# Optimization experiments

Hardware: AMD Instinct MI355X
Metric: run time of the kernel (lower is better)

The kernel has to match this reference:

```python
import jax, jax.numpy as jnp
import numpy as np
from jax import lax

INPUT_DIM = 1024
DICT_SIZE = 16384
K = 32
BATCH = 4096


def setup_inputs() -> dict:
    key = jax.random.key(0)
    k1, k2, k3 = jax.random.split(key, 3)
    x = jax.random.normal(k1, (BATCH, INPUT_DIM), dtype=jnp.float32)
    # kaiming-uniform-ish init for encoder
    bound_enc = float(np.sqrt(6.0 / INPUT_DIM))
    W_enc = jax.random.uniform(k2, (DICT_SIZE, INPUT_DIM), dtype=jnp.float32,
                               minval=-bound_enc, maxval=bound_enc)
    b_enc = jnp.zeros((DICT_SIZE,), dtype=jnp.float32)
    bound_dec = float(np.sqrt(6.0 / DICT_SIZE))
    W_dec = jax.random.uniform(k3, (INPUT_DIM, DICT_SIZE), dtype=jnp.float32,
                               minval=-bound_dec, maxval=bound_dec)
    # normalize decoder columns to unit norm (dim=0), as in _init_weights
    W_dec = W_dec / (jnp.linalg.norm(W_dec, axis=0, keepdims=True) + 1e-12)
    b_dec = jnp.zeros((INPUT_DIM,), dtype=jnp.float32)
    return {"x": x, "W_enc": W_enc, "b_enc": b_enc, "W_dec": W_dec, "b_dec": b_dec}


def reference(x, W_enc, b_enc, W_dec, b_dec):
    batch = x.shape[0]
    # encode: F.linear(x - b_dec, W_enc, b_enc)
    pre_acts = jnp.einsum('bi,di->bd', x - b_dec, W_enc) + b_enc  # [B, D]
    relu_acts = jnp.maximum(pre_acts, 0.0)
    # batch top-k: keep top (k * batch) activations globally
    flat = relu_acts.reshape(-1)
    total_k = min(K * batch, flat.shape[0])
    top_vals, _ = lax.top_k(flat, total_k)
    threshold = top_vals[-1]  # == kthvalue(numel - total_k + 1)
    features = relu_acts * (relu_acts >= threshold).astype(relu_acts.dtype)
    # decode: F.linear(features, W_dec, b_dec)
    reconstructed = jnp.einsum('bd,id->bi', features, W_dec) + b_dec  # [B, I]
    diff = reconstructed - x
    reconstruction_loss = jnp.mean(diff * diff)
    sparsity_loss = jnp.asarray(0.0, dtype=x.dtype)
    loss = reconstruction_loss
    l0 = jnp.mean(jnp.sum((features > 0).astype(jnp.float32), axis=-1))
    return (reconstructed, features, loss, reconstruction_loss, sparsity_loss, l0)
```

## Files before the change

### kernel.cpp

```cpp
#include <hip/hip_runtime.h>
#include <cstdint>
#include <cstddef>

#define BATCH   4096
#define INDIM   1024
#define DICT    16384
#define TOTK    (32 * 4096)
#define NFEAT   ((size_t)BATCH * DICT)
#define DELTA   3e-2f
#define BAND    0.2f
#define PS_RANK (TOTK / 32)

#define NB2       4096
#define FBINS     2048
#define HCOPIES   64
#define CAND_CAP  (1u << 19)
#define BCAP      256u
#define ZLOC_CAP  2048u
#define CLOC_CAP  3072
#define C2_CAP    65536u
#define HASH_SZ   32768u
#define ROW_CAP   512
#define ZBINS     2048

#define PSH_OFF   0ull
#define FH_OFF    16384ull
#define ZHH_OFF   24576ull
#define SCAL_OFF  32768ull
#define H1_OFF    36864ull
#define ROWC_OFF  40960ull
#define HASH_OFF  65536ull
#define FBH_OFF   524288ull
#define MEMSET0   1572864ull
#define CANDI_OFF (2ull << 20)
#define CANDB_OFF (4ull << 20)
#define C2I_OFF   (6ull << 20)
#define C2V_OFF   ((6ull << 20) + 262144)
#define ENT_OFF   (7ull << 20)
#define AHI_OFF   (24ull << 20)
#define BHI_OFF   (32ull << 20)
#define WT_OFF    (24ull << 20)
#define WS_NEED   (88ull << 20)

typedef __attribute__((ext_vector_type(8))) short short8;
typedef __attribute__((ext_vector_type(4))) float f32x4;

#define GL2LDS16(g, l) __builtin_amdgcn_global_load_lds( \
    (const __attribute__((address_space(1))) void*)(g), \
    (__attribute__((address_space(3))) void*)(l), 16, 0, 0)

__device__ inline ushort bf16_rne_u(float a) {
    unsigned u = __float_as_uint(a);
    return (ushort)((u + 0x7FFFu + ((u >> 16) & 1u)) >> 16);
}

__device__ inline int fshift_calc(unsigned BL, unsigned BH) {
    const unsigned range = BH - BL;
    int s = 0;
    while ((range >> s) > (unsigned)FBINS) ++s;
    return s;
}

__global__ __launch_bounds__(256) void split_kernel(
    const float* __restrict__ x, const float* __restrict__ W,
    const float* __restrict__ b_dec,
    ushort* __restrict__ Ahi, ushort* __restrict__ Bhi)
{
    const size_t NA = (size_t)BATCH * INDIM / 4;
    const size_t NB = (size_t)DICT * INDIM / 4;
    const size_t stride = (size_t)gridDim.x * blockDim.x;
    for (size_t i = (size_t)blockIdx.x * blockDim.x + threadIdx.x; i < NA + NB; i += stride) {
        float4 v;
        ushort* hp;
        if (i < NA) {
            v = reinterpret_cast<const float4*>(x)[i];
            const float4 bd = reinterpret_cast<const float4*>(b_dec)[i & (INDIM / 4 - 1)];
            v.x -= bd.x; v.y -= bd.y; v.z -= bd.z; v.w -= bd.w;
            hp = Ahi + i * 4;
        } else {
            v = reinterpret_cast<const float4*>(W)[i - NA];
            hp = Bhi + (i - NA) * 4;
        }
        ushort4 h;
        h.x = bf16_rne_u(v.x);
        h.y = bf16_rne_u(v.y);
        h.z = bf16_rne_u(v.z);
        h.w = bf16_rne_u(v.w);
        *reinterpret_cast<ushort4*>(hp) = h;
    }
}

__global__ __launch_bounds__(256) void presample_mfma(
    const ushort* __restrict__ Ahi, const ushort* __restrict__ Bhi,
    const float* __restrict__ b_enc, unsigned* __restrict__ pshist)
{
    __shared__ __align__(16) ushort As[128 * 64];
    __shared__ __align__(16) ushort Bs[128 * 64];
    __shared__ unsigned hls[NB2];
    const int tid = threadIdx.x;
    const int lane = tid & 63, wid = tid >> 6;
    const int n0 = blockIdx.x * 128;
    const int m0 = 0;
    const int wm = wid >> 1, wn = wid & 1;

    for (int i = tid; i < NB2; i += 256) hls[i] = 0;

    f32x4 acc[4][4];
#pragma unroll
    for (int i = 0; i < 4; ++i)
#pragma unroll
        for (int j = 0; j < 4; ++j) acc[i][j] = (f32x4){0.f, 0.f, 0.f, 0.f};

    const int srow = wid * 8 + (lane >> 3);
    const int schunk = (lane & 7) ^ (lane >> 3);
    const size_t abase = (size_t)(m0 + srow) * INDIM + schunk * 8;
    const size_t bbase = (size_t)(n0 + srow) * INDIM + schunk * 8;

    for (int t = 0; t < 16; ++t) {
        const int koff = t * 64;
#pragma unroll
        for (int i = 0; i < 4; ++i) {
            GL2LDS16(Ahi + abase + koff + (size_t)i * 32 * INDIM, &As[(i * 32 + wid * 8) * 64]);
            GL2LDS16(Bhi + bbase + koff + (size_t)i * 32 * INDIM, &Bs[(i * 32 + wid * 8) * 64]);
        }
        __syncthreads();
#pragma unroll
        for (int kq2 = 0; kq2 < 2; ++kq2) {
            short8 af[4], bf[4];
#pragma unroll
            for (int f = 0; f < 4; ++f) {
                const int ra = wm * 64 + f * 16 + (lane & 15);
                const int ca = (kq2 * 4 + (lane >> 4)) ^ (ra & 7);
                af[f] = *reinterpret_cast<const short8*>(&As[ra * 64 + ca * 8]);
                const int rb = wn * 64 + f * 16 + (lane & 15);
                const int cb = (kq2 * 4 + (lane >> 4)) ^ (rb & 7);
                bf[f] = *reinterpret_cast<const short8*>(&Bs[rb * 64 + cb * 8]);
            }
#pragma unroll
            for (int fm = 0; fm < 4; ++fm)
#pragma unroll
                for (int fn = 0; fn < 4; ++fn)
                    acc[fm][fn] = __builtin_amdgcn_mfma_f32_16x16x32_bf16(
                        af[fm], bf[fn], acc[fm][fn], 0, 0, 0);
        }
        __syncthreads();
    }

    const int ccol0 = n0 + wn * 64;
#pragma unroll
    for (int fm = 0; fm < 4; ++fm) {
#pragma unroll
        for (int fn = 0; fn < 4; ++fn) {
            const int col = ccol0 + fn * 16 + (lane & 15);
            const float be = b_enc[col];
#pragma unroll
            for (int r = 0; r < 4; ++r) {
                const float val = fmaxf(acc[fm][fn][r] + be, 0.f);
                if (val > 0.f) atomicAdd(&hls[__float_as_uint(val) >> 19], 1u);
            }
        }
    }
    __syncthreads();
    for (int i = tid; i < NB2; i += 256)
        if (hls[i]) atomicAdd(&pshist[i], hls[i]);
}

__global__ __launch_bounds__(1024) void presample_find(const unsigned* __restrict__ pshist,
                                                       unsigned* __restrict__ scal)
{
    __shared__ unsigned tot[NB2];
    __shared__ unsigned tsum[1024];
    __shared__ unsigned suffix[1024];
    const int t = threadIdx.x;
    unsigned s = 0;
#pragma unroll
    for (int i = 0; i < 4; ++i) {
        const int b = t * 4 + i;
        const unsigned v = pshist[b];
        tot[b] = v;
        s += v;
    }
    tsum[t] = s;
    __syncthreads();
    if (t == 0) {
        unsigned run = 0;
        for (int i = 1023; i >= 0; --i) { suffix[i] = run; run += tsum[i]; }
    }
    __syncthreads();
    unsigned cum = suffix[t];
    for (int i = 3; i >= 0; --i) {
        const unsigned b = (unsigned)(t * 4 + i);
        const unsigned nb = cum + tot[b];
        if (cum < PS_RANK && nb >= PS_RANK) {
            const float blo = __uint_as_float(b << 19);
            const float bhi = __uint_as_float((b + 1) << 19);
            scal[20] = __float_as_uint(fmaxf(blo - BAND, 1e-30f));
            scal[21] = __float_as_uint(bhi + BAND);
        }
        cum = nb;
    }
}

__global__ __launch_bounds__(256) void encode_main(
    const ushort* __restrict__ Ahi, const ushort* __restrict__ Bhi,
    const float* __restrict__ b_enc, unsigned* __restrict__ scal,
    unsigned* __restrict__ fhist, unsigned* __restrict__ candI,
    unsigned* __restrict__ candB)
{
    __shared__ __align__(16) ushort As[128 * 64];
    __shared__ __align__(16) ushort Bs[128 * 64];
    __shared__ unsigned fh[FBINS];
    __shared__ unsigned ci[BCAP];
    __shared__ unsigned cb[BCAP];
    __shared__ unsigned lcnt, labv, sbase;
    const int tid = threadIdx.x;
    const int lane = tid & 63, wid = tid >> 6;
    const int flat = blockIdx.y * gridDim.x + blockIdx.x;
    const int n0 = ((flat & 7) * 16 + ((flat >> 3) & 15)) * 128;
    const int m0 = (flat >> 7) * 128;
    const int wm = wid >> 1, wn = wid & 1;

    for (int i = tid; i < FBINS; i += 256) fh[i] = 0;
    if (tid == 0) { lcnt = 0; labv = 0; }

    const unsigned BLb = scal[20], BHb = scal[21];
    const float BLf = __uint_as_float(BLb);
    const int fs = fshift_calc(BLb, BHb);

    f32x4 acc[4][4];
#pragma unroll
    for (int i = 0; i < 4; ++i)
#pragma unroll
        for (int j = 0; j < 4; ++j) acc[i][j] = (f32x4){0.f, 0.f, 0.f, 0.f};

    const int srow = wid * 8 + (lane >> 3);
    const int schunk = (lane & 7) ^ (lane >> 3);
    const size_t abase = (size_t)(m0 + srow) * INDIM + schunk * 8;
    const size_t bbase = (size_t)(n0 + srow) * INDIM + schunk * 8;

    for (int t = 0; t < 16; ++t) {
        const int koff = t * 64;
#pragma unroll
        for (int i = 0; i < 4; ++i) {
            GL2LDS16(Ahi + abase + koff + (size_t)i * 32 * INDIM, &As[(i * 32 + wid * 8) * 64]);
            GL2LDS16(Bhi + bbase + koff + (size_t)i * 32 * INDIM, &Bs[(i * 32 + wid * 8) * 64]);
        }
        __syncthreads();
#pragma unroll
        for (int kq2 = 0; kq2 < 2; ++kq2) {
            short8 af[4], bf[4];
#pragma unroll
            for (int f = 0; f < 4; ++f) {
                const int ra = wm * 64 + f * 16 + (lane & 15);
                const int ca = (kq2 * 4 + (lane >> 4)) ^ (ra & 7);
                af[f] = *reinterpret_cast<const short8*>(&As[ra * 64 + ca * 8]);
                const int rb = wn * 64 + f * 16 + (lane & 15);
                const int cbx = (kq2 * 4 + (lane >> 4)) ^ (rb & 7);
                bf[f] = *reinterpret_cast<const short8*>(&Bs[rb * 64 + cbx * 8]);
            }
#pragma unroll
            for (int fm = 0; fm < 4; ++fm)
#pragma unroll
                for (int fn = 0; fn < 4; ++fn)
                    acc[fm][fn] = __builtin_amdgcn_mfma_f32_16x16x32_bf16(
                        af[fm], bf[fn], acc[fm][fn], 0, 0, 0);
        }
        __syncthreads();
    }

    const int crow0 = m0 + wm * 64;
    const int ccol0 = n0 + wn * 64;
#pragma unroll
    for (int fm = 0; fm < 4; ++fm) {
#pragma unroll
        for (int fn = 0; fn < 4; ++fn) {
            const int col = ccol0 + fn * 16 + (lane & 15);
            const float be = b_enc[col];
#pragma unroll
            for (int r = 0; r < 4; ++r) {
                const int row = crow0 + fm * 16 + (lane >> 4) * 4 + r;
                const float val = fmaxf(acc[fm][fn][r] + be, 0.f);
                if (val >= BLf) {
                    const unsigned u = __float_as_uint(val);
                    if (u < BHb) atomicAdd(&fh[min((u - BLb) >> fs, (unsigned)(FBINS - 1))], 1u);
                    else atomicAdd(&labv, 1u);
                    const unsigned p = atomicAdd(&lcnt, 1u);
                    if (p < BCAP) {
                        ci[p] = (unsigned)(row * DICT + col);
                        cb[p] = u;
                    }
                }
            }
        }
    }
    __syncthreads();
    for (int i = tid; i < FBINS; i += 256)
        if (fh[i]) atomicAdd(&fhist[i], fh[i]);
    if (tid == 0) {
        if (labv) atomicAdd(&scal[16], labv);
        const unsigned n = min(lcnt, BCAP);
        if (lcnt > BCAP) atomicExch(&scal[17], 1u);
        sbase = atomicAdd(&scal[2], n);
    }
    __syncthreads();
    const unsigned n = min(lcnt, BCAP);
    const unsigned gb = sbase;
    for (unsigned k = tid; k < n; k += 256) {
        const unsigned g = gb + k;
        if (g < CAND_CAP) { candI[g] = ci[k]; candB[g] = cb[k]; }
        else atomicExch(&scal[17], 1u);
    }
}

__global__ __launch_bounds__(1024) void findfine_a(const unsigned* __restrict__ fhist,
                                                   unsigned* __restrict__ scal)
{
    __shared__ unsigned fhl[FBINS];
    __shared__ unsigned tsum[1024];
    __shared__ unsigned suffix[1024];
    __shared__ unsigned sfb;
    const int t = threadIdx.x;
    fhl[t * 2] = fhist[t * 2];
    fhl[t * 2 + 1] = fhist[t * 2 + 1];
    tsum[t] = fhl[t * 2] + fhl[t * 2 + 1];
    if (t == 0) sfb = 0xFFFFFFFFu;
    __syncthreads();
    if (t == 0) {
        unsigned run = 0;
        for (int i = 1023; i >= 0; --i) { suffix[i] = run; run += tsum[i]; }
    }
    __syncthreads();
    const unsigned aboveBH = scal[16];
    unsigned cum = aboveBH + suffix[t];
    {
        const unsigned b1 = (unsigned)(t * 2 + 1);
        unsigned nb = cum + fhl[b1];
        if (cum < TOTK && nb >= TOTK) sfb = b1;
        cum = nb;
        const unsigned b0 = (unsigned)(t * 2);
        nb = cum + fhl[b0];
        if (cum < TOTK && nb >= TOTK) sfb = b0;
    }
    __syncthreads();
    if (t == 0) {
        const unsigned BLb = scal[20], BHb = scal[21];
        bool ok = (sfb != 0xFFFFFFFFu) && (scal[17] == 0u) && (scal[2] <= CAND_CAP);
        if (ok) {
            const int fs = fshift_calc(BLb, BHb);
            const unsigned flo = BLb + (sfb << fs);
            const unsigned fhi = BLb + ((sfb + 1u) << fs) - 1u;
            const float zLo = __uint_as_float(flo) - DELTA;
            const float zHi = __uint_as_float(fhi) + DELTA;
            const unsigned ZL = __float_as_uint(fmaxf(zLo, 1e-30f));
            const unsigned ZH = __float_as_uint(zHi);
            ok = ok && (ZL >= BLb);
            scal[6] = ZL;
            scal[7] = ZH;
        }
        scal[18] = ok ? 1u : 0u;
    }
}

__global__ __launch_bounds__(256) void findfine_b(const unsigned* __restrict__ candB,
                                                  const unsigned* __restrict__ candI,
                                                  unsigned* __restrict__ scal,
                                                  unsigned* __restrict__ c2idx)
{
    if (!scal[18]) return;
    __shared__ unsigned lz[ZLOC_CAP];
    __shared__ unsigned red[256];
    __shared__ unsigned lcnt, sbase;
    const int tid = threadIdx.x;
    if (tid == 0) lcnt = 0;
    __syncthreads();
    const unsigned ZL = scal[6], ZH = scal[7];
    const unsigned C = min(scal[2], CAND_CAP);
    const unsigned stride = gridDim.x * blockDim.x;
    unsigned above = 0;
    for (unsigned i = blockIdx.x * blockDim.x + tid; i < C; i += stride) {
        const unsigned u = candB[i];
        if (u > ZH) above++;
        else if (u >= ZL) {
            const unsigned p = atomicAdd(&lcnt, 1u);
            if (p < ZLOC_CAP) lz[p] = candI[i];
        }
    }
    red[tid] = above;
    __syncthreads();
    for (int s = 128; s; s >>= 1) {
        if (tid < s) red[tid] += red[tid + s];
        __syncthreads();
    }
    if (tid == 0) {
        if (red[0]) atomicAdd(&scal[8], red[0]);
        const unsigned n = min(lcnt, ZLOC_CAP);
        if (lcnt > ZLOC_CAP) { atomicExch(&scal[17], 1u); atomicExch(&scal[18], 0u); }
        sbase = atomicAdd(&scal[9], n);
    }
    __syncthreads();
    const unsigned n = min(lcnt, ZLOC_CAP);
    const unsigned gb = sbase;
    for (unsigned k = tid; k < n; k += 256) {
        const unsigned g = gb + k;
        if (g < C2_CAP) c2idx[g] = lz[k];
        else { atomicExch(&scal[17], 1u); atomicExch(&scal[18], 0u); }
    }
}

__global__ __launch_bounds__(256) void fb_encode(
    const ushort* __restrict__ Ahi, const ushort* __restrict__ Bhi,
    const float* __restrict__ b_enc, float* __restrict__ feat,
    unsigned* __restrict__ fbhist, const unsigned* __restrict__ scal)
{
    if (scal[18]) return;
    __shared__ __align__(16) ushort As[128 * 64];
    __shared__ __align__(16) ushort Bs[128 * 64];
    __shared__ unsigned hls[NB2];
    const int tid = threadIdx.x;
    const int lane = tid & 63, wid = tid >> 6;
    const int flat = blockIdx.y * gridDim.x + blockIdx.x;
    const int swz = (flat & 7) * 512 + (flat >> 3);
    const int n0 = (swz & 127) * 128;
    const int m0 = (swz >> 7) * 128;
    const int wm = wid >> 1, wn = wid & 1;

    for (int i = tid; i < NB2; i += 256) hls[i] = 0;

    f32x4 acc[4][4];
#pragma unroll
    for (int i = 0; i < 4; ++i)
#pragma unroll
        for (int j = 0; j < 4; ++j) acc[i][j] = (f32x4){0.f, 0.f, 0.f, 0.f};

    const int srow = wid * 8 + (lane >> 3);
    const int schunk = (lane & 7) ^ (lane >> 3);
    const size_t abase = (size_t)(m0 + srow) * INDIM + schunk * 8;
    const size_t bbase = (size_t)(n0 + srow) * INDIM + schunk * 8;

    for (int t = 0; t < 16; ++t) {
        const int koff = t * 64;
#pragma unroll
        for (int i = 0; i < 4; ++i) {
            GL2LDS16(Ahi + abase + koff + (size_t)i * 32 * INDIM, &As[(i * 32 + wid * 8) * 64]);
            GL2LDS16(Bhi + bbase + koff + (size_t)i * 32 * INDIM, &Bs[(i * 32 + wid * 8) * 64]);
        }
        __syncthreads();
#pragma unroll
        for (int kq2 = 0; kq2 < 2; ++kq2) {
            short8 af[4], bf[4];
#pragma unroll
            for (int f = 0; f < 4; ++f) {
                const int ra = wm * 64 + f * 16 + (lane & 15);
                const int ca = (kq2 * 4 + (lane >> 4)) ^ (ra & 7);
                af[f] = *reinterpret_cast<const short8*>(&As[ra * 64 + ca * 8]);
                const int rb = wn * 64 + f * 16 + (lane & 15);
                const int cb = (kq2 * 4 + (lane >> 4)) ^ (rb & 7);
                bf[f] = *reinterpret_cast<const short8*>(&Bs[rb * 64 + cb * 8]);
            }
#pragma unroll
            for (int fm = 0; fm < 4; ++fm)
#pragma unroll
                for (int fn = 0; fn < 4; ++fn)
                    acc[fm][fn] = __builtin_amdgcn_mfma_f32_16x16x32_bf16(
                        af[fm], bf[fn], acc[fm][fn], 0, 0, 0);
        }
        __syncthreads();
    }

    const int crow0 = m0 + wm * 64;
    const int ccol0 = n0 + wn * 64;
#pragma unroll
    for (int fm = 0; fm < 4; ++fm) {
#pragma unroll
        for (int fn = 0; fn < 4; ++fn) {
            const int col = ccol0 + fn * 16 + (lane & 15);
            const float be = b_enc[col];
#pragma unroll
            for (int r = 0; r < 4; ++r) {
                const int row = crow0 + fm * 16 + (lane >> 4) * 4 + r;
                const float val = fmaxf(acc[fm][fn][r] + be, 0.f);
                feat[(size_t)row * DICT + col] = val;
                if (val > 0.f) atomicAdd(&hls[__float_as_uint(val) >> 19], 1u);
            }
        }
    }
    __syncthreads();
    unsigned* hdst = fbhist + (size_t)(flat & (HCOPIES - 1)) * NB2;
    for (int i = tid; i < NB2; i += 256)
        if (hls[i]) atomicAdd(&hdst[i], hls[i]);
}

__global__ __launch_bounds__(1024) void fb_findbin2(const unsigned* __restrict__ fbhist,
                                                    unsigned* __restrict__ scal)
{
    if (scal[18]) return;
    __shared__ unsigned tot[NB2];
    __shared__ unsigned tsum[1024];
    __shared__ unsigned suffix[1024];
    const int t = threadIdx.x;
    if (t == 0) { scal[9] = 0; scal[8] = 0; }
    unsigned s = 0;
#pragma unroll
    for (int i = 0; i < 4; ++i) {
        const int b = t * 4 + i;
        unsigned v = 0;
        for (int c = 0; c < HCOPIES; ++c) v += fbhist[(size_t)c * NB2 + b];
        tot[b] = v;
        s += v;
    }
    tsum[t] = s;
    __syncthreads();
    if (t == 0) {
        unsigned run = 0;
        for (int i = 1023; i >= 0; --i) { suffix[i] = run; run += tsum[i]; }
    }
    __syncthreads();
    unsigned cum = suffix[t];
    for (int i = 3; i >= 0; --i) {
        const unsigned b = (unsigned)(t * 4 + i);
        const unsigned nb = cum + tot[b];
        if (cum < TOTK && nb >= TOTK) {
            scal[0] = b;
            scal[1] = cum;
            scal[10] = cum - ((b + 1 < NB2) ? tot[b + 1] : 0u);
        }
        cum = nb;
    }
}

__global__ __launch_bounds__(256) void fb_collectC(const float* __restrict__ feat,
                                                   unsigned* __restrict__ scal,
                                                   unsigned* __restrict__ candI,
                                                   unsigned* __restrict__ candB,
                                                   unsigned* __restrict__ h1)
{
    if (scal[18]) return;
    __shared__ unsigned lidx[CLOC_CAP];
    __shared__ unsigned lbits[CLOC_CAP];
    __shared__ unsigned lcnt;
    __shared__ unsigned sbase;
    const int tid = threadIdx.x;
    if (tid == 0) lcnt = 0;
    __syncthreads();
    const unsigned b = scal[0];
    const unsigned lob = (b > 0 ? b - 1 : b) << 19;
    const unsigned hib = ((b + 2 < NB2) ? (b + 2) : NB2) << 19;
    const size_t stride = (size_t)gridDim.x * blockDim.x * 4;
    size_t base = ((size_t)blockIdx.x * blockDim.x + tid) * 4;
    for (size_t i = base; i < NFEAT; i += stride) {
        const float4 v = *reinterpret_cast<const float4*>(&feat[i]);
        const unsigned u[4] = {__float_as_uint(v.x), __float_as_uint(v.y),
                               __float_as_uint(v.z), __float_as_uint(v.w)};
#pragma unroll
        for (int q = 0; q < 4; ++q) {
            if (u[q] != 0u && u[q] >= lob && u[q] < hib) {
                const unsigned p = atomicAdd(&lcnt, 1u);
                if (p < CLOC_CAP) { lidx[p] = (unsigned)(i + q); lbits[p] = u[q]; }
                if ((u[q] >> 19) == b) atomicAdd(&h1[(u[q] >> 9) & 1023u], 1u);
            }
        }
    }
    __syncthreads();
    const unsigned n = min(lcnt, (unsigned)CLOC_CAP);
    if (tid == 0) sbase = atomicAdd(&scal[24], n);
    __syncthreads();
    const unsigned gb = sbase;
    for (unsigned k = tid; k < n; k += 256) {
        const unsigned g = gb + k;
        if (g < CAND_CAP) { candI[g] = lidx[k]; candB[g] = lbits[k]; }
    }
}

__global__ __launch_bounds__(1024) void fb_selectZ(const unsigned* __restrict__ h1,
                                                   const unsigned* __restrict__ candB,
                                                   const unsigned* __restrict__ candI,
                                                   unsigned* __restrict__ scal,
                                                   unsigned* __restrict__ c2idx)
{
    if (scal[18]) return;
    __shared__ unsigned h[1024];
    __shared__ unsigned cnt[1024];
    const int t = threadIdx.x;
    h[t] = h1[t];
    __syncthreads();
    if (t == 0) {
        const unsigned b = scal[0];
        unsigned cum = scal[1];
        unsigned s = 0;
        for (int i = 1023; i >= 0; --i) {
            const unsigned nb = cum + h[i];
            if (cum < TOTK && nb >= TOTK) s = (unsigned)i;
            cum = nb;
        }
        const float slo = __uint_as_float((b << 19) | (s << 9));
        const float shi = __uint_as_float((b << 19) | (s << 9) | 0x1FFu);
        scal[6] = __float_as_uint(fmaxf(slo - DELTA, 1e-30f));
        scal[7] = __float_as_uint(shi + DELTA);
    }
    __syncthreads();
    const float ZLf = __uint_as_float(scal[6]);
    const float ZHf = __uint_as_float(scal[7]);
    const unsigned C = min(scal[24], CAND_CAP);
    unsigned above = 0;
    for (unsigned i = t; i < C; i += 1024) {
        const float v = __uint_as_float(candB[i]);
        if (v > ZHf) above++;
        else if (v >= ZLf) {
            const unsigned p = atomicAdd(&scal[9], 1u);
            if (p < C2_CAP) c2idx[p] = candI[i];
        }
    }
    cnt[t] = above;
    __syncthreads();
    for (int s2 = 512; s2; s2 >>= 1) {
        if (t < s2) cnt[t] += cnt[t + s2];
        __syncthreads();
    }
    if (t == 0) scal[8] = scal[10] + cnt[0];
}

__global__ __launch_bounds__(256) void refine2_kernel(
    const float* __restrict__ x, const float* __restrict__ W,
    const float* __restrict__ b_enc, const float* __restrict__ b_dec,
    const unsigned* __restrict__ scal, const unsigned* __restrict__ c2idx,
    float* __restrict__ c2val)
{
    const unsigned n = min(scal[9], C2_CAP);
    const size_t stride = (size_t)gridDim.x * blockDim.x;
    for (unsigned c = blockIdx.x * blockDim.x + threadIdx.x; c < n; c += stride) {
        const unsigned i = c2idx[c];
        const int m = (int)(i >> 14);
        const int d = (int)(i & (DICT - 1));
        const float* xr = x + (size_t)m * INDIM;
        const float* wr = W + (size_t)d * INDIM;
        const int kb[4] = {0, 384, 704, 1024};
        float tot = 0.f;
        for (int p = 0; p < 3; ++p) {
            float a = 0.f;
#pragma unroll 8
            for (int k = kb[p]; k < kb[p + 1]; ++k)
                a = fmaf(xr[k] - b_dec[k], wr[k], a);
            tot = (p == 0) ? a : (tot + a);
        }
        c2val[c] = tot + b_enc[d];
    }
}

__device__ inline int zone_shift(unsigned ZL, unsigned ZH) {
    const unsigned range = ZH - ZL + 1u;
    int shift = 0;
    while ((range >> shift) > (unsigned)ZBINS) ++shift;
    return shift;
}

__global__ __launch_bounds__(256) void zhist_kernel(const unsigned* __restrict__ scal,
                                                    const float* __restrict__ c2val,
                                                    unsigned* __restrict__ zh)
{
    __shared__ unsigned h[ZBINS];
    for (int i = threadIdx.x; i < ZBINS; i += 256) h[i] = 0;
    __syncthreads();
    const unsigned n = min(scal[9], C2_CAP);
    const unsigned ZL = scal[6], ZH = scal[7];
    const int shift = zone_shift(ZL, ZH);
    const unsigned stride = gridDim.x * blockDim.x;
    for (unsigned i = blockIdx.x * blockDim.x + threadIdx.x; i < n; i += stride) {
        const unsigned bits = __float_as_uint(c2val[i]);
        const unsigned idx = (bits <= ZL) ? 0u : min((unsigned)(ZBINS - 1), (bits - ZL) >> shift);
        atomicAdd(&h[idx], 1u);
    }
    __syncthreads();
    for (int i = threadIdx.x; i < ZBINS; i += 256)
        if (h[i]) atomicAdd(&zh[i], h[i]);
}

__global__ __launch_bounds__(1024) void findv_kernel(const unsigned* __restrict__ zh,
                                                     const float* __restrict__ c2val,
                                                     unsigned* __restrict__ scal)
{
    __shared__ unsigned h[ZBINS];
    __shared__ float mem[1024];
    __shared__ unsigned mcnt;
    __shared__ unsigned sbsel, sjj;
    const int t = threadIdx.x;
    h[t] = zh[t];
    h[t + 1024] = zh[t + 1024];
    if (t == 0) mcnt = 0;
    __syncthreads();
    const unsigned n = min(scal[9], C2_CAP);
    unsigned j = TOTK - scal[8];
    if (j > n) j = n;
    if (t == 0) {
        unsigned cum = 0, bsel = 0, jj = j;
        for (int i = ZBINS - 1; i >= 0; --i) {
            const unsigned nb = cum + h[i];
            if (cum < j && nb >= j) { bsel = (unsigned)i; jj = j - cum; }
            cum = nb;
        }
        sbsel = bsel; sjj = jj;
    }
    __syncthreads();
    const unsigned ZL = scal[6], ZH = scal[7];
    const int shift = zone_shift(ZL, ZH);
    const unsigned bsel = sbsel, jj = sjj;
    for (unsigned i = t; i < n; i += 1024) {
        const unsigned bits = __float_as_uint(c2val[i]);
        const unsigned idx = (bits <= ZL) ? 0u : min((unsigned)(ZBINS - 1), (bits - ZL) >> shift);
        if (idx == bsel) {
            const unsigned p = atomicAdd(&mcnt, 1u);
            if (p < 1024) mem[p] = c2val[i];
        }
    }
    __syncthreads();
    const unsigned m = min(mcnt, 1024u);
    for (unsigned i = t; i < m; i += 1024) {
        const float v = mem[i];
        unsigned g = 0, eq = 0;
        for (unsigned d = 0; d < m; ++d) {
            g += (mem[d] > v) ? 1u : 0u;
            eq += (mem[d] == v) ? 1u : 0u;
        }
        if (g < jj && g + eq >= jj) scal[11] = __float_as_uint(v);
    }
}

__global__ __launch_bounds__(256) void keephash_kernel(const unsigned* __restrict__ scal,
                                                       const unsigned* __restrict__ c2idx,
                                                       const float* __restrict__ c2val,
                                                       uint2* __restrict__ hash)
{
    const unsigned n = min(scal[9], C2_CAP);
    const float vj = __uint_as_float(scal[11]);
    const unsigned stride = gridDim.x * blockDim.x;
    for (unsigned i = blockIdx.x * blockDim.x + threadIdx.x; i < n; i += stride) {
        const float v = c2val[i];
        if (v >= vj) {
            const unsigned key = c2idx[i];
            unsigned s = (key * 2654435761u) & (HASH_SZ - 1);
            while (atomicCAS(&hash[s].x, 0xFFFFFFFFu, key) != 0xFFFFFFFFu)
                s = (s + 1) & (HASH_SZ - 1);
            hash[s].y = __float_as_uint(v);
        }
    }
}

__global__ void transpose_kernel(const float* __restrict__ W, float* __restrict__ Wt)
{
    __shared__ float t[32][33];
    const int x0 = blockIdx.x * 32;
    const int y0 = blockIdx.y * 32;
    const int tx = threadIdx.x, ty = threadIdx.y;
    for (int r = ty; r < 32; r += 8)
        t[r][tx] = W[(size_t)(y0 + r) * DICT + x0 + tx];
    __syncthreads();
    for (int r = ty; r < 32; r += 8)
        Wt[(size_t)(x0 + r) * INDIM + y0 + tx] = t[tx][r];
}

__global__ __launch_bounds__(256) void scatter_kernel(
    unsigned* __restrict__ scal, const unsigned* __restrict__ candI,
    const unsigned* __restrict__ candB, const uint2* __restrict__ hash,
    float* __restrict__ feat, uint2* __restrict__ entries,
    unsigned* __restrict__ rowcnt)
{
    if (!scal[18]) return;
    __shared__ unsigned red[256];
    const unsigned C = min(scal[2], CAND_CAP);
    const unsigned ZL = scal[6], ZH = scal[7];
    const unsigned stride = gridDim.x * blockDim.x;
    unsigned kept = 0;
    for (unsigned i = blockIdx.x * blockDim.x + threadIdx.x; i < C; i += stride) {
        const unsigned u = candB[i];
        const unsigned idx = candI[i];
        float val = 0.f;
        bool keep = false;
        if (u > ZH) {
            val = __uint_as_float(u);
            keep = true;
        } else if (u >= ZL) {
            unsigned s = (idx * 2654435761u) & (HASH_SZ - 1);
            while (true) {
                const uint2 e = hash[s];
                if (e.x == idx) { val = __uint_as_float(e.y); keep = true; break; }
                if (e.x == 0xFFFFFFFFu) break;
                s = (s + 1) & (HASH_SZ - 1);
            }
        }
        if (keep) {
            feat[idx] = val;
            const unsigned row = idx >> 14;
            const unsigned p = atomicAdd(&rowcnt[row], 1u);
            if (p < ROW_CAP)
                entries[(size_t)row * ROW_CAP + p] =
                    make_uint2(idx & (DICT - 1), __float_as_uint(val));
            kept++;
        }
    }
    red[threadIdx.x] = kept;
    __syncthreads();
    for (int s = 128; s; s >>= 1) {
        if (threadIdx.x < s) red[threadIdx.x] += red[threadIdx.x + s];
        __syncthreads();
    }
    if (threadIdx.x == 0 && red[0]) atomicAdd(&scal[4], red[0]);
}

__global__ __launch_bounds__(256) void decode2_kernel(
    const unsigned* __restrict__ scal, const uint2* __restrict__ entries,
    const unsigned* __restrict__ rowcnt, const float* __restrict__ Wt,
    const float* __restrict__ b_dec, const float* __restrict__ x,
    float* __restrict__ recon, double* __restrict__ loss_sum)
{
    if (!scal[18]) return;
    __shared__ uint2 lst[ROW_CAP];
    __shared__ double redd[256];
    const int row = blockIdx.x;
    const int tid = threadIdx.x;
    const unsigned n = min(rowcnt[row], (unsigned)ROW_CAP);
    for (unsigned i = tid; i < n; i += 256) lst[i] = entries[(size_t)row * ROW_CAP + i];
    __syncthreads();
    float4 acc = make_float4(0.f, 0.f, 0.f, 0.f);
    for (unsigned e = 0; e < n; ++e) {
        const uint2 en = lst[e];
        const float v = __uint_as_float(en.y);
        const float4 w = *reinterpret_cast<const float4*>(Wt + (size_t)en.x * INDIM + tid * 4);
        acc.x = fmaf(v, w.x, acc.x);
        acc.y = fmaf(v, w.y, acc.y);
        acc.z = fmaf(v, w.z, acc.z);
        acc.w = fmaf(v, w.w, acc.w);
    }
    const float4 bd = reinterpret_cast<const float4*>(b_dec)[tid];
    acc.x += bd.x; acc.y += bd.y; acc.z += bd.z; acc.w += bd.w;
    reinterpret_cast<float4*>(recon + (size_t)row * INDIM)[tid] = acc;
    const float4 xv = reinterpret_cast<const float4*>(x + (size_t)row * INDIM)[tid];
    const double d0 = (double)acc.x - (double)xv.x;
    const double d1 = (double)acc.y - (double)xv.y;
    const double d2 = (double)acc.z - (double)xv.z;
    const double d3 = (double)acc.w - (double)xv.w;
    redd[tid] = d0 * d0 + d1 * d1 + d2 * d2 + d3 * d3;
    __syncthreads();
    for (int s = 128; s; s >>= 1) {
        if (tid < s) redd[tid] += redd[tid + s];
        __syncthreads();
    }
    if (tid == 0) atomicAdd(loss_sum, redd[0]);
}

__global__ __launch_bounds__(256) void fb_compact_decode(
    float* __restrict__ feat, unsigned* __restrict__ scal,
    const uint2* __restrict__ hash, const float* __restrict__ Wt,
    const float* __restrict__ b_dec, const float* __restrict__ x,
    float* __restrict__ recon, double* __restrict__ loss_sum)
{
    if (scal[18]) return;
    __shared__ uint2 lst[ROW_CAP];
    __shared__ unsigned cnt;
    __shared__ double redd[256];
    const int row = blockIdx.x;
    const int tid = threadIdx.x;
    if (tid == 0) cnt = 0;
    __syncthreads();
    const float ZLf = __uint_as_float(scal[6]);
    const float ZHf = __uint_as_float(scal[7]);
    float* frow = feat + (size_t)row * DICT;
#pragma unroll
    for (int it = 0; it < DICT / 4 / 256; ++it) {
        const int i4 = it * 256 + tid;
        float4 v = reinterpret_cast<float4*>(frow)[i4];
        float a[4] = {v.x, v.y, v.z, v.w};
        float out[4] = {0.f, 0.f, 0.f, 0.f};
#pragma unroll
        for (int q = 0; q < 4; ++q) {
            const float val = a[q];
            if (val > ZHf) {
                out[q] = val;
            } else if (val >= ZLf && val > 0.f) {
                const unsigned key = (unsigned)(row * DICT + i4 * 4 + q);
                unsigned s = (key * 2654435761u) & (HASH_SZ - 1);
                while (true) {
                    const uint2 e = hash[s];
                    if (e.x == key) { out[q] = __uint_as_float(e.y); break; }
                    if (e.x == 0xFFFFFFFFu) break;
                    s = (s + 1) & (HASH_SZ - 1);
                }
            }
            if (out[q] != 0.f) {
                const unsigned p = atomicAdd(&cnt, 1u);
                if (p < ROW_CAP)
                    lst[p] = make_uint2((unsigned)(i4 * 4 + q), __float_as_uint(out[q]));
            }
        }
        reinterpret_cast<float4*>(frow)[i4] = make_float4(out[0], out[1], out[2], out[3]);
    }
    __syncthreads();
    const unsigned n = min(cnt, (unsigned)ROW_CAP);
    float4 acc = make_float4(0.f, 0.f, 0.f, 0.f);
    for (unsigned e = 0; e < n; ++e) {
        const uint2 en = lst[e];
        const float v = __uint_as_float(en.y);
        const float4 w = *reinterpret_cast<const float4*>(Wt + (size_t)en.x * INDIM + tid * 4);
        acc.x = fmaf(v, w.x, acc.x);
        acc.y = fmaf(v, w.y, acc.y);
        acc.z = fmaf(v, w.z, acc.z);
        acc.w = fmaf(v, w.w, acc.w);
    }
    const float4 bd = reinterpret_cast<const float4*>(b_dec)[tid];
    acc.x += bd.x; acc.y += bd.y; acc.z += bd.z; acc.w += bd.w;
    reinterpret_cast<float4*>(recon + (size_t)row * INDIM)[tid] = acc;
    const float4 xv = reinterpret_cast<const float4*>(x + (size_t)row * INDIM)[tid];
    const double d0 = (double)acc.x - (double)xv.x;
    const double d1 = (double)acc.y - (double)xv.y;
    const double d2 = (double)acc.z - (double)xv.z;
    const double d3 = (double)acc.w - (double)xv.w;
    redd[tid] = d0 * d0 + d1 * d1 + d2 * d2 + d3 * d3;
    __syncthreads();
    for (int s = 128; s; s >>= 1) {
        if (tid < s) redd[tid] += redd[tid + s];
        __syncthreads();
    }
    if (tid == 0) {
        atomicAdd(loss_sum, redd[0]);
        if (cnt) atomicAdd(&scal[4], cnt);
    }
}

__global__ void finalize_kernel(const unsigned* __restrict__ scal, float* __restrict__ tail)
{
    const double* loss_d = reinterpret_cast<const double*>(&scal[12]);
    const float rec = (float)(loss_d[0] / (double)((size_t)BATCH * INDIM));
    tail[0] = rec;
    tail[1] = rec;
    tail[2] = 0.f;
    tail[3] = (float)scal[4] / (float)BATCH;
}

extern "C" void kernel_launch(void* const* d_in, const int* in_sizes, int n_in,
                              void* d_out, int out_size, void* d_ws, size_t ws_size,
                              hipStream_t stream)
{
    const float* x     = (const float*)d_in[0];
    const float* W_enc = (const float*)d_in[1];
    const float* b_enc = (const float*)d_in[2];
    const float* W_dec = (const float*)d_in[3];
    const float* b_dec = (const float*)d_in[4];

    float* recon = (float*)d_out;
    float* feat  = recon + (size_t)BATCH * INDIM;
    float* tail  = feat + NFEAT;

    unsigned* pshist = (unsigned*)((char*)d_ws + PSH_OFF);
    unsigned* fhist  = (unsigned*)((char*)d_ws + FH_OFF);
    unsigned* zh     = (unsigned*)((char*)d_ws + ZHH_OFF);
    unsigned* scal   = (unsigned*)((char*)d_ws + SCAL_OFF);
    unsigned* h1     = (unsigned*)((char*)d_ws + H1_OFF);
    unsigned* rowcnt = (unsigned*)((char*)d_ws + ROWC_OFF);
    uint2*    hash   = (uint2*)   ((char*)d_ws + HASH_OFF);
    unsigned* fbhist = (unsigned*)((char*)d_ws + FBH_OFF);
    unsigned* candI  = (unsigned*)((char*)d_ws + CANDI_OFF);
    unsigned* candB  = (unsigned*)((char*)d_ws + CANDB_OFF);
    unsigned* c2idx  = (unsigned*)((char*)d_ws + C2I_OFF);
    float*    c2val  = (float*)   ((char*)d_ws + C2V_OFF);
    uint2*    entries= (uint2*)   ((char*)d_ws + ENT_OFF);
    ushort*   Ahi    = (ushort*)  ((char*)d_ws + AHI_OFF);
    ushort*   Bhi    = (ushort*)  ((char*)d_ws + BHI_OFF);
    float*    Wt     = (float*)   ((char*)d_ws + WT_OFF);
    double*   loss_sum = (double*)&scal[12];

    hipMemsetAsync(d_ws, 0, MEMSET0, stream);
    hipMemsetAsync((char*)d_ws + HASH_OFF, 0xFF, HASH_SZ * sizeof(uint2), stream);
    hipMemsetAsync(feat, 0, NFEAT * sizeof(float), stream);

    split_kernel<<<2048, 256, 0, stream>>>(x, W_enc, b_dec, Ahi, Bhi);
    presample_mfma<<<128, 256, 0, stream>>>(Ahi, Bhi, b_enc, pshist);
    presample_find<<<1, 1024, 0, stream>>>(pshist, scal);
    encode_main<<<dim3(128, 32), 256, 0, stream>>>(Ahi, Bhi, b_enc, scal, fhist, candI, candB);
    findfine_a<<<1, 1024, 0, stream>>>(fhist, scal);
    findfine_b<<<256, 256, 0, stream>>>(candB, candI, scal, c2idx);

    fb_encode<<<dim3(128, 32), 256, 0, stream>>>(Ahi, Bhi, b_enc, feat, fbhist, scal);
    fb_findbin2<<<1, 1024, 0, stream>>>(fbhist, scal);
    fb_collectC<<<1024, 256, 0, stream>>>(feat, scal, candI, candB, h1);
    fb_selectZ<<<1, 1024, 0, stream>>>(h1, candB, candI, scal, c2idx);

    refine2_kernel<<<128, 256, 0, stream>>>(x, W_enc, b_enc, b_dec, scal, c2idx, c2val);
    zhist_kernel<<<32, 256, 0, stream>>>(scal, c2val, zh);
    findv_kernel<<<1, 1024, 0, stream>>>(zh, c2val, scal);
    keephash_kernel<<<64, 256, 0, stream>>>(scal, c2idx, c2val, hash);

    transpose_kernel<<<dim3(DICT / 32, INDIM / 32), dim3(32, 8), 0, stream>>>(W_dec, Wt);

    scatter_kernel<<<256, 256, 0, stream>>>(scal, candI, candB, hash, feat, entries, rowcnt);
    decode2_kernel<<<BATCH, 256, 0, stream>>>(scal, entries, rowcnt, Wt, b_dec, x, recon, loss_sum);
    fb_compact_decode<<<BATCH, 256, 0, stream>>>(feat, scal, hash, Wt, b_dec, x, recon, loss_sum);

    finalize_kernel<<<1, 1, 0, stream>>>(scal, tail);
}
```

Before: 629.4 us.

## Store decoder weights as bf16, fold zone histogram into findv, use global fhist atomics

The transposed decoder weight matrix is now stored as bf16 instead of fp32, which halves transpose write traffic and the gather reads in both decode kernels, at the cost of decoder precision. The separate zhist kernel is removed and its histogram is built inside the single-block findv kernel, saving one launch. encode_main drops its shared-memory fine histogram and does atomics straight into the global fhist. That reduces LDS use but may add contention on global atomics.

```diff
diff --git a/kernel.cpp b/kernel.cpp
--- a/kernel.cpp
+++ b/kernel.cpp
@@ -25,7 +25,6 @@
 
 #define PSH_OFF   0ull
 #define FH_OFF    16384ull
-#define ZHH_OFF   24576ull
 #define SCAL_OFF  32768ull
 #define H1_OFF    36864ull
 #define ROWC_OFF  40960ull
@@ -54,6 +53,10 @@
     return (ushort)((u + 0x7FFFu + ((u >> 16) & 1u)) >> 16);
 }
 
+__device__ inline float bf16_to_f(ushort u) {
+    return __uint_as_float(((unsigned)u) << 16);
+}
+
 __device__ inline int fshift_calc(unsigned BL, unsigned BH) {
     const unsigned range = BH - BL;
     int s = 0;
@@ -209,7 +212,6 @@
 {
     __shared__ __align__(16) ushort As[128 * 64];
     __shared__ __align__(16) ushort Bs[128 * 64];
-    __shared__ unsigned fh[FBINS];
     __shared__ unsigned ci[BCAP];
     __shared__ unsigned cb[BCAP];
     __shared__ unsigned lcnt, labv, sbase;
@@ -220,7 +222,6 @@
     const int m0 = (flat >> 7) * 128;
     const int wm = wid >> 1, wn = wid & 1;
 
-    for (int i = tid; i < FBINS; i += 256) fh[i] = 0;
     if (tid == 0) { lcnt = 0; labv = 0; }
 
     const unsigned BLb = scal[20], BHb = scal[21];
@@ -282,7 +283,7 @@
                 const float val = fmaxf(acc[fm][fn][r] + be, 0.f);
                 if (val >= BLf) {
                     const unsigned u = __float_as_uint(val);
-                    if (u < BHb) atomicAdd(&fh[min((u - BLb) >> fs, (unsigned)(FBINS - 1))], 1u);
+                    if (u < BHb) atomicAdd(&fhist[min((u - BLb) >> fs, (unsigned)(FBINS - 1))], 1u);
                     else atomicAdd(&labv, 1u);
                     const unsigned p = atomicAdd(&lcnt, 1u);
                     if (p < BCAP) {
@@ -294,8 +295,6 @@
         }
     }
     __syncthreads();
-    for (int i = tid; i < FBINS; i += 256)
-        if (fh[i]) atomicAdd(&fhist[i], fh[i]);
     if (tid == 0) {
         if (labv) atomicAdd(&scal[16], labv);
         const unsigned n = min(lcnt, BCAP);
@@ -653,29 +652,7 @@
     return shift;
 }
 
-__global__ __launch_bounds__(256) void zhist_kernel(const unsigned* __restrict__ scal,
-                                                    const float* __restrict__ c2val,
-                                                    unsigned* __restrict__ zh)
-{
-    __shared__ unsigned h[ZBINS];
-    for (int i = threadIdx.x; i < ZBINS; i += 256) h[i] = 0;
-    __syncthreads();
-    const unsigned n = min(scal[9], C2_CAP);
-    const unsigned ZL = scal[6], ZH = scal[7];
-    const int shift = zone_shift(ZL, ZH);
-    const unsigned stride = gridDim.x * blockDim.x;
-    for (unsigned i = blockIdx.x * blockDim.x + threadIdx.x; i < n; i += stride) {
-        const unsigned bits = __float_as_uint(c2val[i]);
-        const unsigned idx = (bits <= ZL) ? 0u : min((unsigned)(ZBINS - 1), (bits - ZL) >> shift);
-        atomicAdd(&h[idx], 1u);
-    }
-    __syncthreads();
-    for (int i = threadIdx.x; i < ZBINS; i += 256)
-        if (h[i]) atomicAdd(&zh[i], h[i]);
-}
-
-__global__ __launch_bounds__(1024) void findv_kernel(const unsigned* __restrict__ zh,
-                                                     const float* __restrict__ c2val,
+__global__ __launch_bounds__(1024) void findv_kernel(const float* __restrict__ c2val,
                                                      unsigned* __restrict__ scal)
 {
     __shared__ unsigned h[ZBINS];
@@ -683,11 +660,19 @@
     __shared__ unsigned mcnt;
     __shared__ unsigned sbsel, sjj;
     const int t = threadIdx.x;
-    h[t] = zh[t];
-    h[t + 1024] = zh[t + 1024];
+    h[t] = 0;
+    h[t + 1024] = 0;
     if (t == 0) mcnt = 0;
     __syncthreads();
     const unsigned n = min(scal[9], C2_CAP);
+    const unsigned ZL = scal[6], ZH = scal[7];
+    const int shift = zone_shift(ZL, ZH);
+    for (unsigned i = t; i < n; i += 1024) {
+        const unsigned bits = __float_as_uint(c2val[i]);
+        const unsigned idx = (bits <= ZL) ? 0u : min((unsigned)(ZBINS - 1), (bits - ZL) >> shift);
+        atomicAdd(&h[idx], 1u);
+    }
+    __syncthreads();
     unsigned j = TOTK - scal[8];
     if (j > n) j = n;
     if (t == 0) {
@@ -700,8 +685,6 @@
         sbsel = bsel; sjj = jj;
     }
     __syncthreads();
-    const unsigned ZL = scal[6], ZH = scal[7];
-    const int shift = zone_shift(ZL, ZH);
     const unsigned bsel = sbsel, jj = sjj;
     for (unsigned i = t; i < n; i += 1024) {
         const unsigned bits = __float_as_uint(c2val[i]);
@@ -744,7 +727,7 @@
     }
 }
 
-__global__ void transpose_kernel(const float* __restrict__ W, float* __restrict__ Wt)
+__global__ void transpose_kernel(const float* __restrict__ W, ushort* __restrict__ Wt)
 {
     __shared__ float t[32][33];
     const int x0 = blockIdx.x * 32;
@@ -754,7 +737,7 @@
         t[r][tx] = W[(size_t)(y0 + r) * DICT + x0 + tx];
     __syncthreads();
     for (int r = ty; r < 32; r += 8)
-        Wt[(size_t)(x0 + r) * INDIM + y0 + tx] = t[tx][r];
+        Wt[(size_t)(x0 + r) * INDIM + y0 + tx] = bf16_rne_u(t[tx][r]);
 }
 
 __global__ __launch_bounds__(256) void scatter_kernel(
@@ -807,7 +790,7 @@
 
 __global__ __launch_bounds__(256) void decode2_kernel(
     const unsigned* __restrict__ scal, const uint2* __restrict__ entries,
-    const unsigned* __restrict__ rowcnt, const float* __restrict__ Wt,
+    const unsigned* __restrict__ rowcnt, const ushort* __restrict__ Wt,
     const float* __restrict__ b_dec, const float* __restrict__ x,
     float* __restrict__ recon, double* __restrict__ loss_sum)
 {
@@ -823,11 +806,11 @@
     for (unsigned e = 0; e < n; ++e) {
         const uint2 en = lst[e];
         const float v = __uint_as_float(en.y);
-        const float4 w = *reinterpret_cast<const float4*>(Wt + (size_t)en.x * INDIM + tid * 4);
-        acc.x = fmaf(v, w.x, acc.x);
-        acc.y = fmaf(v, w.y, acc.y);
-        acc.z = fmaf(v, w.z, acc.z);
-        acc.w = fmaf(v, w.w, acc.w);
+        const ushort4 w4 = *reinterpret_cast<const ushort4*>(Wt + (size_t)en.x * INDIM + tid * 4);
+        acc.x = fmaf(v, bf16_to_f(w4.x), acc.x);
+        acc.y = fmaf(v, bf16_to_f(w4.y), acc.y);
+        acc.z = fmaf(v, bf16_to_f(w4.z), acc.z);
+        acc.w = fmaf(v, bf16_to_f(w4.w), acc.w);
     }
     const float4 bd = reinterpret_cast<const float4*>(b_dec)[tid];
     acc.x += bd.x; acc.y += bd.y; acc.z += bd.z; acc.w += bd.w;
@@ -848,7 +831,7 @@
 
 __global__ __launch_bounds__(256) void fb_compact_decode(
     float* __restrict__ feat, unsigned* __restrict__ scal,
-    const uint2* __restrict__ hash, const float* __restrict__ Wt,
+    const uint2* __restrict__ hash, const ushort* __restrict__ Wt,
     const float* __restrict__ b_dec, const float* __restrict__ x,
     float* __restrict__ recon, double* __restrict__ loss_sum)
 {
@@ -898,11 +881,11 @@
     for (unsigned e = 0; e < n; ++e) {
         const uint2 en = lst[e];
         const float v = __uint_as_float(en.y);
-        const float4 w = *reinterpret_cast<const float4*>(Wt + (size_t)en.x * INDIM + tid * 4);
-        acc.x = fmaf(v, w.x, acc.x);
-        acc.y = fmaf(v, w.y, acc.y);
-        acc.z = fmaf(v, w.z, acc.z);
-        acc.w = fmaf(v, w.w, acc.w);
+        const ushort4 w4 = *reinterpret_cast<const ushort4*>(Wt + (size_t)en.x * INDIM + tid * 4);
+        acc.x = fmaf(v, bf16_to_f(w4.x), acc.x);
+        acc.y = fmaf(v, bf16_to_f(w4.y), acc.y);
+        acc.z = fmaf(v, bf16_to_f(w4.z), acc.z);
+        acc.w = fmaf(v, bf16_to_f(w4.w), acc.w);
     }
     const float4 bd = reinterpret_cast<const float4*>(b_dec)[tid];
     acc.x += bd.x; acc.y += bd.y; acc.z += bd.z; acc.w += bd.w;
@@ -950,7 +933,6 @@
 
     unsigned* pshist = (unsigned*)((char*)d_ws + PSH_OFF);
     unsigned* fhist  = (unsigned*)((char*)d_ws + FH_OFF);
-    unsigned* zh     = (unsigned*)((char*)d_ws + ZHH_OFF);
     unsigned* scal   = (unsigned*)((char*)d_ws + SCAL_OFF);
     unsigned* h1     = (unsigned*)((char*)d_ws + H1_OFF);
     unsigned* rowcnt = (unsigned*)((char*)d_ws + ROWC_OFF);
@@ -963,7 +945,7 @@
     uint2*    entries= (uint2*)   ((char*)d_ws + ENT_OFF);
     ushort*   Ahi    = (ushort*)  ((char*)d_ws + AHI_OFF);
     ushort*   Bhi    = (ushort*)  ((char*)d_ws + BHI_OFF);
-    float*    Wt     = (float*)   ((char*)d_ws + WT_OFF);
+    ushort*   Wt     = (ushort*)  ((char*)d_ws + WT_OFF);
     double*   loss_sum = (double*)&scal[12];
 
     hipMemsetAsync(d_ws, 0, MEMSET0, stream);
@@ -983,8 +965,7 @@
     fb_selectZ<<<1, 1024, 0, stream>>>(h1, candB, candI, scal, c2idx);
 
     refine2_kernel<<<128, 256, 0, stream>>>(x, W_enc, b_enc, b_dec, scal, c2idx, c2val);
-    zhist_kernel<<<32, 256, 0, stream>>>(scal, c2val, zh);
-    findv_kernel<<<1, 1024, 0, stream>>>(zh, c2val, scal);
+    findv_kernel<<<1, 1024, 0, stream>>>(c2val, scal);
     keephash_kernel<<<64, 256, 0, stream>>>(scal, c2idx, c2val, hash);
 
     transpose_kernel<<<dim3(DICT / 32, INDIM / 32), dim3(32, 8), 0, stream>>>(W_dec, Wt);
```

Measured after the change: 606.7 us. 3.6% less time.
